# Kernel tuning notes

Hardware: AMD Instinct MI355X
Metric: run time of the kernel (lower is better)

## Reference

```python
import jax, jax.numpy as jnp
import numpy as np

N_HEADS = 12


def setup_inputs() -> dict:
    key = jax.random.key(0)
    ks = jax.random.split(key, 4)
    B, S, D = 2, 2048, 768
    x = jax.random.normal(ks[0], (B, S, D), dtype=jnp.float32)
    # nn.Linear-style init scale ~ 1/sqrt(D) to keep logits reasonable
    scale = 1.0 / np.sqrt(D)
    Wq = jax.random.normal(ks[1], (D, D), dtype=jnp.float32) * scale
    Wk = jax.random.normal(ks[2], (D, D), dtype=jnp.float32) * scale
    Wv = jax.random.normal(ks[3], (D, D), dtype=jnp.float32) * scale
    bq = jnp.zeros((D,), jnp.float32)
    bk = jnp.zeros((D,), jnp.float32)
    bv = jnp.zeros((D,), jnp.float32)
    mask = jnp.ones((B, S), jnp.int32)
    return {"x": x, "Wq": Wq, "bq": bq, "Wk": Wk, "bk": bk,
            "Wv": Wv, "bv": bv, "mask": mask}


def reference(x, Wq, bq, Wk, bk, Wv, bv, mask):
    B, S, D = x.shape
    H = N_HEADS
    W = D // H
    # q,k,v: (B,S,D) -> (B,H,S,W)
    def proj(Wm, bm):
        return (x @ Wm.T + bm).reshape(B, S, H, W).transpose(0, 2, 1, 3)
    q, k, v = proj(Wq, bq), proj(Wk, bk), proj(Wv, bv)
    scores = jnp.einsum("bhsw,bhtw->bhst", q, k) / jnp.sqrt(
        jnp.asarray(W, x.dtype))
    # mask: (B,S) -> broadcast over query positions; 0 -> -1e20
    scores = jnp.where(mask[:, None, None, :] == 0,
                       jnp.asarray(-1e20, scores.dtype), scores)
    attn = jax.nn.softmax(scores, axis=-1)  # (B,H,S,S)
    # dropout p=0.0 (eval) -> identity
    ctx = jnp.einsum("bhst,bhtw->bhsw", attn, v)
    hidden = ctx.transpose(0, 2, 1, 3).reshape(B, S, D)
    return hidden
```

## Files before the change

### kernel.cpp

```cpp
#include <hip/hip_runtime.h>
#include <hip/hip_bf16.h>
#include <stdint.h>


typedef __attribute__((ext_vector_type(8))) short bf16x8;
typedef __attribute__((ext_vector_type(4))) float f32x4;
typedef __attribute__((ext_vector_type(16))) float f32x16;
typedef __attribute__((ext_vector_type(8))) unsigned short u16x8;

#define MFMA16(a, b, c) __builtin_amdgcn_mfma_f32_16x16x32_bf16((a), (b), (c), 0, 0, 0)
#define MFMA32(a, b, c) __builtin_amdgcn_mfma_f32_32x32x16_bf16((a), (b), (c), 0, 0, 0)
#define SWZ(row, colb) ((colb) ^ (((row) & 7) << 4))

union U32x4BF {
  unsigned u[4];
  bf16x8 v;
};

__device__ __forceinline__ void gl_lds16(const void* g, void* l) {
  __builtin_amdgcn_global_load_lds(
      (__attribute__((address_space(1))) void*)const_cast<void*>(g),
      (__attribute__((address_space(3))) void*)l, 16, 0, 0);
}

__device__ __forceinline__ unsigned short f2bf(float x) {
  unsigned int v = __float_as_uint(x);
  return (unsigned short)((v + 0x7fffu + ((v >> 16) & 1u)) >> 16);
}

__global__ __launch_bounds__(256) void cvt_all(
    const float* __restrict__ x, const float* __restrict__ wq,
    const float* __restrict__ wk, const float* __restrict__ wv,
    unsigned short* __restrict__ xb, unsigned short* __restrict__ wb) {
  int i = blockIdx.x * 256 + threadIdx.x;
  const float* s;
  unsigned short* d;
  int off;
  if (i < 393216)      { s = x;  d = xb;            off = i; }
  else if (i < 466944) { s = wq; d = wb;            off = i - 393216; }
  else if (i < 540672) { s = wk; d = wb + 589824;   off = i - 466944; }
  else                 { s = wv; d = wb + 1179648;  off = i - 540672; }
  const float4* sp = (const float4*)s + (size_t)off * 2;
  float4 a = sp[0], b2 = sp[1];
  u16x8 o;
  o[0] = f2bf(a.x); o[1] = f2bf(a.y); o[2] = f2bf(a.z); o[3] = f2bf(a.w);
  o[4] = f2bf(b2.x); o[5] = f2bf(b2.y); o[6] = f2bf(b2.z); o[7] = f2bf(b2.w);
  *((u16x8*)d + off) = o;
}

__global__ __launch_bounds__(256) void proj_gemm(
    const unsigned short* __restrict__ xb, const unsigned short* __restrict__ wb,
    const float* __restrict__ bq, const float* __restrict__ bk, const float* __restrict__ bv,
    unsigned short* __restrict__ qw, unsigned short* __restrict__ kw,
    unsigned short* __restrict__ vw) {
  __shared__ __align__(16) char psmem[49152];
  const int t = threadIdx.x, lane = t & 63, wave = t >> 6;
  const int lo = lane & 15, hi = lane >> 4;
  const int wr = wave >> 1, wc = wave & 1;
  const int mbase = blockIdx.x * 128;
  const int wsel = blockIdx.y / 6;
  const int nbase = (blockIdx.y % 6) * 128;
  const char* xc = (const char*)xb;
  const char* wmc = (const char*)(wb + (size_t)wsel * 589824);

  const int pp0 = t * 16, pp1 = t * 16 + 4096;
  const int ar0 = pp0 >> 7, ac0 = (pp0 & 127) ^ ((ar0 & 7) << 4);
  const int am0 = ((ac0 >> 6) << 6) + ar0, ak0 = ac0 & 63;
  const int ar1 = pp1 >> 7, ac1 = (pp1 & 127) ^ ((ar1 & 7) << 4);
  const int am1 = ((ac1 >> 6) << 6) + ar1, ak1 = ac1 & 63;

#define PSTAGE(IT, BUF)                                                          \
  do {                                                                           \
    int it_ = (IT);                                                              \
    char* lb = psmem + (BUF) * 16384;                                            \
    gl_lds16(xc + (size_t)(mbase + am0) * 1536 + it_ * 64 + ak0, lb + pp0);      \
    gl_lds16(xc + (size_t)(mbase + am1) * 1536 + it_ * 64 + ak1, lb + pp1);      \
    gl_lds16(wmc + (size_t)(nbase + am0) * 1536 + it_ * 64 + ak0, lb + 8192 + pp0); \
    gl_lds16(wmc + (size_t)(nbase + am1) * 1536 + it_ * 64 + ak1, lb + 8192 + pp1); \
  } while (0)

  f32x4 acc[4][4];
#pragma unroll
  for (int i = 0; i < 4; i++)
#pragma unroll
    for (int j = 0; j < 4; j++) acc[i][j] = (f32x4){0.f, 0.f, 0.f, 0.f};

  const int axor = (lo & 7) << 4;
  PSTAGE(0, 0);
  int cur = 0, nxt = 1;
  for (int it = 0; it < 24; ++it) {
    if (it < 23) {
      PSTAGE(it + 1, nxt);
      asm volatile("s_waitcnt vmcnt(4)" ::: "memory");
    } else {
      asm volatile("s_waitcnt vmcnt(0)" ::: "memory");
    }
    __builtin_amdgcn_s_barrier();
    const char* lA = psmem + cur * 16384;
    const char* lB = lA + 8192;

    bf16x8 af[4], bf[4];
#pragma unroll
    for (int mf = 0; mf < 4; mf++)
      af[mf] = *(const bf16x8*)(lA + (mf * 16 + lo) * 128 + ((wr * 64 + hi * 16) ^ axor));
#pragma unroll
    for (int nf = 0; nf < 4; nf++)
      bf[nf] = *(const bf16x8*)(lB + (nf * 16 + lo) * 128 + ((wc * 64 + hi * 16) ^ axor));

    __builtin_amdgcn_s_setprio(1);
    if (wsel == 2) {
#pragma unroll
      for (int mf = 0; mf < 4; mf++)
#pragma unroll
        for (int nf = 0; nf < 4; nf++) acc[mf][nf] = MFMA16(bf[nf], af[mf], acc[mf][nf]);
    } else {
#pragma unroll
      for (int mf = 0; mf < 4; mf++)
#pragma unroll
        for (int nf = 0; nf < 4; nf++) acc[mf][nf] = MFMA16(af[mf], bf[nf], acc[mf][nf]);
    }
    __builtin_amdgcn_s_setprio(0);
    cur = nxt;
    nxt = (nxt == 2) ? 0 : nxt + 1;
  }
#undef PSTAGE

  const float QSCALE = 0.125f * 1.44269504089f;
  if (wsel == 2) {
#pragma unroll
    for (int nf = 0; nf < 4; nf++) {
#pragma unroll
      for (int mf = 0; mf < 4; mf++) {
#pragma unroll
        for (int r = 0; r < 4; r++) {
          int n = nbase + wc * 64 + nf * 16 + hi * 4 + r;
          int m = mbase + wr * 64 + mf * 16 + lo;
          int b_ = m >> 11, s = m & 2047;
          int h = n >> 6, wcol = n & 63;
          float val = acc[mf][nf][r] + bv[n];
          vw[(((size_t)b_ * 12 + h) * 64 + wcol) * 2048 + s] = f2bf(val);
        }
      }
    }
  } else {
    const float* bias = (wsel == 0) ? bq : bk;
#pragma unroll
    for (int nf = 0; nf < 4; nf++) {
      int n = nbase + wc * 64 + nf * 16 + lo;
      float bv_ = bias[n];
      int h = n >> 6, wcol = n & 63;
#pragma unroll
      for (int mf = 0; mf < 4; mf++) {
#pragma unroll
        for (int r = 0; r < 4; r++) {
          int m = mbase + wr * 64 + mf * 16 + hi * 4 + r;
          int b_ = m >> 11, s = m & 2047;
          float val = acc[mf][nf][r] + bv_;
          size_t bhh = (size_t)b_ * 12 + h;
          if (wsel == 0)
            qw[(bhh * 2048 + s) * 64 + wcol] = f2bf(val * QSCALE);
          else
            kw[(bhh * 2048 + s) * 64 + wcol] = f2bf(val);
        }
      }
    }
  }
}

__global__ __launch_bounds__(256) void attn_kernel(
    const unsigned short* __restrict__ qw, const unsigned short* __restrict__ kw,
    const unsigned short* __restrict__ vw, const int* __restrict__ mask,
    float* __restrict__ out) {
  __shared__ __align__(16) char smem[49920];
  const int t = threadIdx.x, lane = t & 63, wave = t >> 6;
  const int wq = wave >> 1, wk = wave & 1;
  const int l31 = lane & 31, hl = lane >> 5;
  const int qb = blockIdx.x, bh = blockIdx.y;
  const int b = bh / 12, hh = bh - b * 12;

  {
    const int* mb = mask + (size_t)b * 2048 + t * 8;
    int4 a0 = *(const int4*)mb;
    int4 a1 = *(const int4*)(mb + 4);
    unsigned by = (unsigned)(a0.x != 0) | ((unsigned)(a0.y != 0) << 1) |
                  ((unsigned)(a0.z != 0) << 2) | ((unsigned)(a0.w != 0) << 3) |
                  ((unsigned)(a1.x != 0) << 4) | ((unsigned)(a1.y != 0) << 5) |
                  ((unsigned)(a1.z != 0) << 6) | ((unsigned)(a1.w != 0) << 7);
    smem[49152 + t] = (char)by;
  }
  asm volatile("s_waitcnt lgkmcnt(0)" ::: "memory");

  bf16x8 qv[4];
  {
    int qrow = qb * 64 + wq * 32 + l31;
    const char* qp = (const char*)qw + ((size_t)bh * 2048 + qrow) * 128 + hl * 16;
#pragma unroll
    for (int s = 0; s < 4; s++) qv[s] = *(const bf16x8*)(qp + s * 32);
  }

  const char* kbaseg = (const char*)kw + (size_t)bh * 262144;
  const char* vbaseg = (const char*)vw + (size_t)bh * 262144;

  const int p0 = t * 16, p1 = t * 16 + 4096;
  const int r0 = p0 >> 9, c0 = (p0 >> 7) & 3, o0 = (p0 & 127) ^ ((r0 & 7) << 4);
  const int ks0 = (c0 * 16 + r0) * 128 + o0, vs0 = (c0 * 16 + r0) * 4096 + o0;
  const int r1 = p1 >> 9, c1 = (p1 >> 7) & 3, o1 = (p1 & 127) ^ ((r1 & 7) << 4);
  const int ks1 = (c1 * 16 + r1) * 128 + o1, vs1 = (c1 * 16 + r1) * 4096 + o1;

#define STAGE(IT, BUF)                                                     \
  do {                                                                     \
    int it_ = (IT);                                                        \
    char* kb = smem + (BUF) * 16384;                                       \
    gl_lds16(kbaseg + (size_t)it_ * 8192 + ks0, kb + p0);                  \
    gl_lds16(kbaseg + (size_t)it_ * 8192 + ks1, kb + p1);                  \
    gl_lds16(vbaseg + (size_t)it_ * 128 + vs0, kb + 8192 + p0);            \
    gl_lds16(vbaseg + (size_t)it_ * 128 + vs1, kb + 8192 + p1);            \
  } while (0)

  f32x16 oacc[2];
#pragma unroll
  for (int wh = 0; wh < 2; wh++)
#pragma unroll
    for (int g = 0; g < 16; g++) oacc[wh][g] = 0.f;
  float lacc = 0.f;

  const int kbl = (l31 & 15) * 512 + (wk * 2 + (l31 >> 4)) * 128;
  const int rxor = (l31 & 7) << 4;
  const int hl16 = hl * 16;

  STAGE(0, 0);
  int cur = 0, nxt = 1;
  for (int it = 0; it < 32; ++it) {
    if (it < 31) {
      STAGE(it + 1, nxt);
      asm volatile("s_waitcnt vmcnt(4)" ::: "memory");
    } else {
      asm volatile("s_waitcnt vmcnt(0)" ::: "memory");
    }
    __builtin_amdgcn_s_barrier();

    const char* lKc = smem + cur * 16384;
    const char* lVc = lKc + 8192;

    f32x16 sc;
#pragma unroll
    for (int g = 0; g < 16; g++) sc[g] = 0.f;
    __builtin_amdgcn_s_setprio(1);
#pragma unroll
    for (int s = 0; s < 4; s++) {
      bf16x8 kf = *(const bf16x8*)(lKc + kbl + ((s * 32 + hl16) ^ rxor));
      sc = MFMA32(kf, qv[s], sc);
    }
    __builtin_amdgcn_s_setprio(0);

    unsigned long long bal = *(const unsigned long long*)(smem + 49152 + it * 8);
    if (bal != ~0ull) {
#pragma unroll
      for (int g = 0; g < 16; g++) {
        int key = wk * 32 + 4 * hl + (g & 3) + 8 * (g >> 2);
        if (!((bal >> key) & 1)) sc[g] = -30000.f;
      }
    }

    float e[16];
#pragma unroll
    for (int g = 0; g < 16; g++)
      asm("v_exp_f32 %0, %1" : "=v"(e[g]) : "v"(sc[g]));
    lacc += (((e[0] + e[1]) + (e[2] + e[3])) + ((e[4] + e[5]) + (e[6] + e[7]))) +
            (((e[8] + e[9]) + (e[10] + e[11])) + ((e[12] + e[13]) + (e[14] + e[15])));
    unsigned pk[4][2];
#pragma unroll
    for (int m = 0; m < 4; m++) {
      asm("v_cvt_pk_bf16_f32 %0, %1, %2" : "=v"(pk[m][0]) : "v"(e[4 * m]), "v"(e[4 * m + 1]));
      asm("v_cvt_pk_bf16_f32 %0, %1, %2" : "=v"(pk[m][1]) : "v"(e[4 * m + 2]), "v"(e[4 * m + 3]));
    }
    U32x4BF apv[2];
#pragma unroll
    for (int sp = 0; sp < 2; sp++)
#pragma unroll
      for (int cp = 0; cp < 2; cp++) {
        unsigned xx = pk[2 * sp][cp], yy = pk[2 * sp + 1][cp];
        asm("v_permlane32_swap_b32 %0, %1" : "+v"(xx), "+v"(yy));
        apv[sp].u[cp] = xx;
        apv[sp].u[2 + cp] = yy;
      }

    __builtin_amdgcn_s_setprio(1);
#pragma unroll
    for (int wh = 0; wh < 2; wh++) {
      int vbl = (l31 & 15) * 512 + (wh * 2 + (l31 >> 4)) * 128;
#pragma unroll
      for (int sp = 0; sp < 2; sp++) {
        bf16x8 vf = *(const bf16x8*)(lVc + vbl + ((wk * 64 + sp * 32 + hl16) ^ rxor));
        oacc[wh] = MFMA32(apv[sp].v, vf, oacc[wh]);
      }
    }
    __builtin_amdgcn_s_setprio(0);
    cur = nxt;
    nxt = (nxt == 2) ? 0 : nxt + 1;
  }

  lacc += __shfl_xor(lacc, 32);
  if (lane < 32)
    *(float*)(smem + 49408 + (wk * 64 + wq * 32 + l31) * 4) = lacc;
  if (wk == 1) {
#pragma unroll
    for (int wh = 0; wh < 2; wh++) {
      int vrow = wh * 32 + l31;
#pragma unroll
      for (int m = 0; m < 4; m++) {
        f32x4 part = (f32x4){oacc[wh][4 * m], oacc[wh][4 * m + 1],
                             oacc[wh][4 * m + 2], oacc[wh][4 * m + 3]};
        *(f32x4*)(smem + wq * 8192 + vrow * 128 + SWZ(vrow, hl * 16 + m * 32)) = part;
      }
    }
  }
  __syncthreads();
  if (wk == 0) {
    float linv[16];
#pragma unroll
    for (int g = 0; g < 16; g++) {
      int qrow = 4 * hl + (g & 3) + 8 * (g >> 2);
      float l0 = *(const float*)(smem + 49408 + (wq * 32 + qrow) * 4);
      float l1 = *(const float*)(smem + 49408 + (64 + wq * 32 + qrow) * 4);
      linv[g] = __builtin_amdgcn_rcpf(l0 + l1);
    }
#pragma unroll
    for (int wh = 0; wh < 2; wh++) {
      int vrow = wh * 32 + l31;
#pragma unroll
      for (int m = 0; m < 4; m++) {
        f32x4 part = *(const f32x4*)(smem + wq * 8192 + vrow * 128 + SWZ(vrow, hl * 16 + m * 32));
#pragma unroll
        for (int r = 0; r < 4; r++) {
          int g = 4 * m + r;
          int qrow = 4 * hl + r + 8 * m;
          float val = (oacc[wh][g] + part[r]) * linv[g];
          out[((size_t)b * 2048 + qb * 64 + wq * 32 + qrow) * 768 + hh * 64 + wh * 32 + l31] =
              val;
        }
      }
    }
  }
#undef STAGE
}

extern "C" void kernel_launch(void* const* d_in, const int* in_sizes, int n_in,
                              void* d_out, int out_size, void* d_ws, size_t ws_size,
                              hipStream_t stream) {
  (void)in_sizes; (void)n_in; (void)out_size; (void)ws_size;
  const float* x  = (const float*)d_in[0];
  const float* Wq = (const float*)d_in[1];
  const float* bq = (const float*)d_in[2];
  const float* Wk = (const float*)d_in[3];
  const float* bk = (const float*)d_in[4];
  const float* Wv = (const float*)d_in[5];
  const float* bv = (const float*)d_in[6];
  const int* mask = (const int*)d_in[7];
  float* out = (float*)d_out;

  char* ws = (char*)d_ws;
  unsigned short* xb = (unsigned short*)(ws);
  unsigned short* wb = (unsigned short*)(ws + 6291456);
  unsigned short* qw = (unsigned short*)(ws + 9830400);
  unsigned short* kw = (unsigned short*)(ws + 16121856);
  unsigned short* vw = (unsigned short*)(ws + 22413312);

  cvt_all<<<2400, 256, 0, stream>>>(x, Wq, Wk, Wv, xb, wb);
  proj_gemm<<<dim3(32, 18), 256, 0, stream>>>(xb, wb, bq, bk, bv, qw, kw, vw);
  attn_kernel<<<dim3(32, 24), 256, 0, stream>>>(qw, kw, vw, mask, out);
}
```

Measured before the change: 86.74 us.

## Deepen prefetch to two stages and compute softmax row sums via MFMA

Both the projection GEMM and the attention kernel now prefetch two tiles ahead in a three-buffer ring, with pointer-increment addressing and an extra barrier at the end of each iteration to protect buffer reuse. The attention loop is manually unrolled by three so buffer indices are compile-time constants. Per-row softmax denominators are now accumulated with an MFMA against a ones vector instead of 16 scalar adds plus a cross-lane shuffle. The aim is to hide more load latency and move VALU work onto the matrix unit, at the cost of an extra barrier per iteration and bf16-rounded exponentials in the denominator sum.

```diff
diff --git a/kernel.cpp b/kernel.cpp
--- a/kernel.cpp
+++ b/kernel.cpp
@@ -69,14 +69,19 @@
   const int ar1 = pp1 >> 7, ac1 = (pp1 & 127) ^ ((ar1 & 7) << 4);
   const int am1 = ((ac1 >> 6) << 6) + ar1, ak1 = ac1 & 63;
 
-#define PSTAGE(IT, BUF)                                                          \
-  do {                                                                           \
-    int it_ = (IT);                                                              \
-    char* lb = psmem + (BUF) * 16384;                                            \
-    gl_lds16(xc + (size_t)(mbase + am0) * 1536 + it_ * 64 + ak0, lb + pp0);      \
-    gl_lds16(xc + (size_t)(mbase + am1) * 1536 + it_ * 64 + ak1, lb + pp1);      \
-    gl_lds16(wmc + (size_t)(nbase + am0) * 1536 + it_ * 64 + ak0, lb + 8192 + pp0); \
-    gl_lds16(wmc + (size_t)(nbase + am1) * 1536 + it_ * 64 + ak1, lb + 8192 + pp1); \
+  const char* xa0 = xc + (size_t)(mbase + am0) * 1536 + ak0;
+  const char* xa1 = xc + (size_t)(mbase + am1) * 1536 + ak1;
+  const char* wa0 = wmc + (size_t)(nbase + am0) * 1536 + ak0;
+  const char* wa1 = wmc + (size_t)(nbase + am1) * 1536 + ak1;
+
+#define PSTAGE(BUF)                              \
+  do {                                           \
+    char* lb = psmem + (BUF) * 16384;            \
+    gl_lds16(xa0, lb + pp0);                     \
+    gl_lds16(xa1, lb + pp1);                     \
+    gl_lds16(wa0, lb + 8192 + pp0);              \
+    gl_lds16(wa1, lb + 8192 + pp1);              \
+    xa0 += 64; xa1 += 64; wa0 += 64; wa1 += 64;  \
   } while (0)
 
   f32x4 acc[4][4];
@@ -86,11 +91,15 @@
     for (int j = 0; j < 4; j++) acc[i][j] = (f32x4){0.f, 0.f, 0.f, 0.f};
 
   const int axor = (lo & 7) << 4;
-  PSTAGE(0, 0);
-  int cur = 0, nxt = 1;
+  PSTAGE(0);
+  PSTAGE(1);
+  int cur = 0, sb = 2;
+#pragma unroll 1
   for (int it = 0; it < 24; ++it) {
-    if (it < 23) {
-      PSTAGE(it + 1, nxt);
+    if (it < 22) {
+      PSTAGE(sb);
+      asm volatile("s_waitcnt vmcnt(8)" ::: "memory");
+    } else if (it == 22) {
       asm volatile("s_waitcnt vmcnt(4)" ::: "memory");
     } else {
       asm volatile("s_waitcnt vmcnt(0)" ::: "memory");
@@ -120,8 +129,9 @@
         for (int nf = 0; nf < 4; nf++) acc[mf][nf] = MFMA16(af[mf], bf[nf], acc[mf][nf]);
     }
     __builtin_amdgcn_s_setprio(0);
-    cur = nxt;
-    nxt = (nxt == 2) ? 0 : nxt + 1;
+    __builtin_amdgcn_s_barrier();
+    cur = (cur == 2) ? 0 : cur + 1;
+    sb = (sb == 2) ? 0 : sb + 1;
   }
 #undef PSTAGE
 
@@ -171,7 +181,7 @@
     const unsigned short* __restrict__ qw, const unsigned short* __restrict__ kw,
     const unsigned short* __restrict__ vw, const int* __restrict__ mask,
     float* __restrict__ out) {
-  __shared__ __align__(16) char smem[49920];
+  __shared__ __align__(16) char smem[49664];
   const int t = threadIdx.x, lane = t & 63, wave = t >> 6;
   const int wq = wave >> 1, wk = wave & 1;
   const int l31 = lane & 31, hl = lane >> 5;
@@ -198,112 +208,116 @@
     for (int s = 0; s < 4; s++) qv[s] = *(const bf16x8*)(qp + s * 32);
   }
 
-  const char* kbaseg = (const char*)kw + (size_t)bh * 262144;
-  const char* vbaseg = (const char*)vw + (size_t)bh * 262144;
-
   const int p0 = t * 16, p1 = t * 16 + 4096;
   const int r0 = p0 >> 9, c0 = (p0 >> 7) & 3, o0 = (p0 & 127) ^ ((r0 & 7) << 4);
-  const int ks0 = (c0 * 16 + r0) * 128 + o0, vs0 = (c0 * 16 + r0) * 4096 + o0;
   const int r1 = p1 >> 9, c1 = (p1 >> 7) & 3, o1 = (p1 & 127) ^ ((r1 & 7) << 4);
-  const int ks1 = (c1 * 16 + r1) * 128 + o1, vs1 = (c1 * 16 + r1) * 4096 + o1;
-
-#define STAGE(IT, BUF)                                                     \
-  do {                                                                     \
-    int it_ = (IT);                                                        \
-    char* kb = smem + (BUF) * 16384;                                       \
-    gl_lds16(kbaseg + (size_t)it_ * 8192 + ks0, kb + p0);                  \
-    gl_lds16(kbaseg + (size_t)it_ * 8192 + ks1, kb + p1);                  \
-    gl_lds16(vbaseg + (size_t)it_ * 128 + vs0, kb + 8192 + p0);            \
-    gl_lds16(vbaseg + (size_t)it_ * 128 + vs1, kb + 8192 + p1);            \
+
+  const char* kp0 = (const char*)kw + (size_t)bh * 262144 + (c0 * 16 + r0) * 128 + o0;
+  const char* kp1 = (const char*)kw + (size_t)bh * 262144 + (c1 * 16 + r1) * 128 + o1;
+  const char* vp0 = (const char*)vw + (size_t)bh * 262144 + (size_t)(c0 * 16 + r0) * 4096 + o0;
+  const char* vp1 = (const char*)vw + (size_t)bh * 262144 + (size_t)(c1 * 16 + r1) * 4096 + o1;
+
+#define STAGEP(BUF_)                              \
+  do {                                            \
+    char* kb_ = smem + (BUF_) * 16384;            \
+    gl_lds16(kp0, kb_ + p0);                      \
+    gl_lds16(kp1, kb_ + p1);                      \
+    gl_lds16(vp0, kb_ + 8192 + p0);               \
+    gl_lds16(vp1, kb_ + 8192 + p1);               \
+    kp0 += 8192; kp1 += 8192; vp0 += 128; vp1 += 128; \
   } while (0)
 
-  f32x16 oacc[2];
+  f32x16 oacc[2], lsacc;
 #pragma unroll
   for (int wh = 0; wh < 2; wh++)
 #pragma unroll
     for (int g = 0; g < 16; g++) oacc[wh][g] = 0.f;
-  float lacc = 0.f;
+#pragma unroll
+  for (int g = 0; g < 16; g++) lsacc[g] = 0.f;
+  U32x4BF onesv;
+  onesv.u[0] = onesv.u[1] = onesv.u[2] = onesv.u[3] = 0x3F803F80u;
 
   const int kbl = (l31 & 15) * 512 + (wk * 2 + (l31 >> 4)) * 128;
   const int rxor = (l31 & 7) << 4;
   const int hl16 = hl * 16;
 
-  STAGE(0, 0);
-  int cur = 0, nxt = 1;
-  for (int it = 0; it < 32; ++it) {
-    if (it < 31) {
-      STAGE(it + 1, nxt);
-      asm volatile("s_waitcnt vmcnt(4)" ::: "memory");
-    } else {
-      asm volatile("s_waitcnt vmcnt(0)" ::: "memory");
-    }
-    __builtin_amdgcn_s_barrier();
-
-    const char* lKc = smem + cur * 16384;
-    const char* lVc = lKc + 8192;
-
-    f32x16 sc;
-#pragma unroll
-    for (int g = 0; g < 16; g++) sc[g] = 0.f;
-    __builtin_amdgcn_s_setprio(1);
-#pragma unroll
-    for (int s = 0; s < 4; s++) {
-      bf16x8 kf = *(const bf16x8*)(lKc + kbl + ((s * 32 + hl16) ^ rxor));
-      sc = MFMA32(kf, qv[s], sc);
-    }
-    __builtin_amdgcn_s_setprio(0);
-
-    unsigned long long bal = *(const unsigned long long*)(smem + 49152 + it * 8);
-    if (bal != ~0ull) {
+  STAGEP(0);
+  STAGEP(1);
+
+#define BODY(IT_, BUF_, DOSTAGE_, SBUF_, VMW_)                                         \
+  {                                                                                    \
+    if (DOSTAGE_) STAGEP(SBUF_);                                                       \
+    asm volatile("s_waitcnt vmcnt(" #VMW_ ")" ::: "memory");                           \
+    __builtin_amdgcn_s_barrier();                                                      \
+    const char* lKc_ = smem + (BUF_) * 16384;                                          \
+    const char* lVc_ = lKc_ + 8192;                                                    \
+    f32x16 sc_;                                                                        \
+    _Pragma("unroll") for (int g = 0; g < 16; g++) sc_[g] = 0.f;                       \
+    __builtin_amdgcn_s_setprio(1);                                                     \
+    _Pragma("unroll") for (int s = 0; s < 4; s++) {                                    \
+      bf16x8 kf_ = *(const bf16x8*)(lKc_ + kbl + ((s * 32 + hl16) ^ rxor));            \
+      sc_ = MFMA32(kf_, qv[s], sc_);                                                   \
+    }                                                                                  \
+    __builtin_amdgcn_s_setprio(0);                                                     \
+    unsigned long long bal_ = *(const unsigned long long*)(smem + 49152 + (IT_) * 8);  \
+    if (bal_ != ~0ull) {                                                               \
+      _Pragma("unroll") for (int g = 0; g < 16; g++) {                                 \
+        int key_ = wk * 32 + 4 * hl + (g & 3) + 8 * (g >> 2);                          \
+        if (!((bal_ >> key_) & 1)) sc_[g] = -30000.f;                                  \
+      }                                                                                \
+    }                                                                                  \
+    float e_[16];                                                                      \
+    _Pragma("unroll") for (int g = 0; g < 16; g++)                                     \
+        asm("v_exp_f32 %0, %1" : "=v"(e_[g]) : "v"(sc_[g]));                           \
+    unsigned pk_[4][2];                                                                \
+    _Pragma("unroll") for (int m = 0; m < 4; m++) {                                    \
+      asm("v_cvt_pk_bf16_f32 %0, %1, %2"                                               \
+          : "=v"(pk_[m][0]) : "v"(e_[4 * m]), "v"(e_[4 * m + 1]));                     \
+      asm("v_cvt_pk_bf16_f32 %0, %1, %2"                                               \
+          : "=v"(pk_[m][1]) : "v"(e_[4 * m + 2]), "v"(e_[4 * m + 3]));                 \
+    }                                                                                  \
+    U32x4BF apv_[2];                                                                   \
+    _Pragma("unroll") for (int sp = 0; sp < 2; sp++)                                   \
+        _Pragma("unroll") for (int cp = 0; cp < 2; cp++) {                             \
+      unsigned xx_ = pk_[2 * sp][cp], yy_ = pk_[2 * sp + 1][cp];                       \
+      asm("v_permlane32_swap_b32 %0, %1" : "+v"(xx_), "+v"(yy_));                      \
+      apv_[sp].u[cp] = xx_;                                                            \
+      apv_[sp].u[2 + cp] = yy_;                                                        \
+    }                                                                                  \
+    __builtin_amdgcn_s_setprio(1);                                                     \
+    lsacc = MFMA32(apv_[0].v, onesv.v, lsacc);                                         \
+    lsacc = MFMA32(apv_[1].v, onesv.v, lsacc);                                         \
+    _Pragma("unroll") for (int wh = 0; wh < 2; wh++) {                                 \
+      int vbl_ = (l31 & 15) * 512 + (wh * 2 + (l31 >> 4)) * 128;                       \
+      _Pragma("unroll") for (int sp = 0; sp < 2; sp++) {                               \
+        bf16x8 vf_ =                                                                   \
+            *(const bf16x8*)(lVc_ + vbl_ + ((wk * 64 + sp * 32 + hl16) ^ rxor));       \
+        oacc[wh] = MFMA32(apv_[sp].v, vf_, oacc[wh]);                                  \
+      }                                                                                \
+    }                                                                                  \
+    __builtin_amdgcn_s_setprio(0);                                                     \
+    __builtin_amdgcn_s_barrier();         \
+  }
+
+#pragma unroll 1
+  for (int itb = 0; itb < 30; itb += 3) {
+    BODY(itb, 0, 1, 2, 8);
+    BODY(itb + 1, 1, 1, 0, 8);
+    BODY(itb + 2, 2, 1, 1, 8);
+  }
+  BODY(30, 0, 0, 0, 4);
+  BODY(31, 1, 0, 0, 0);
+#undef BODY
+#undef STAGEP
+
+  if (wk == 1) {
+    if (l31 == 0) {
 #pragma unroll
       for (int g = 0; g < 16; g++) {
-        int key = wk * 32 + 4 * hl + (g & 3) + 8 * (g >> 2);
-        if (!((bal >> key) & 1)) sc[g] = -30000.f;
-      }
-    }
-
-    float e[16];
-#pragma unroll
-    for (int g = 0; g < 16; g++)
-      asm("v_exp_f32 %0, %1" : "=v"(e[g]) : "v"(sc[g]));
-    lacc += (((e[0] + e[1]) + (e[2] + e[3])) + ((e[4] + e[5]) + (e[6] + e[7]))) +
-            (((e[8] + e[9]) + (e[10] + e[11])) + ((e[12] + e[13]) + (e[14] + e[15])));
-    unsigned pk[4][2];
-#pragma unroll
-    for (int m = 0; m < 4; m++) {
-      asm("v_cvt_pk_bf16_f32 %0, %1, %2" : "=v"(pk[m][0]) : "v"(e[4 * m]), "v"(e[4 * m + 1]));
-      asm("v_cvt_pk_bf16_f32 %0, %1, %2" : "=v"(pk[m][1]) : "v"(e[4 * m + 2]), "v"(e[4 * m + 3]));
-    }
-    U32x4BF apv[2];
-#pragma unroll
-    for (int sp = 0; sp < 2; sp++)
-#pragma unroll
-      for (int cp = 0; cp < 2; cp++) {
-        unsigned xx = pk[2 * sp][cp], yy = pk[2 * sp + 1][cp];
-        asm("v_permlane32_swap_b32 %0, %1" : "+v"(xx), "+v"(yy));
-        apv[sp].u[cp] = xx;
-        apv[sp].u[2 + cp] = yy;
-      }
-
-    __builtin_amdgcn_s_setprio(1);
-#pragma unroll
-    for (int wh = 0; wh < 2; wh++) {
-      int vbl = (l31 & 15) * 512 + (wh * 2 + (l31 >> 4)) * 128;
-#pragma unroll
-      for (int sp = 0; sp < 2; sp++) {
-        bf16x8 vf = *(const bf16x8*)(lVc + vbl + ((wk * 64 + sp * 32 + hl16) ^ rxor));
-        oacc[wh] = MFMA32(apv[sp].v, vf, oacc[wh]);
-      }
-    }
-    __builtin_amdgcn_s_setprio(0);
-    cur = nxt;
-    nxt = (nxt == 2) ? 0 : nxt + 1;
-  }
-
-  lacc += __shfl_xor(lacc, 32);
-  if (lane < 32)
-    *(float*)(smem + 49408 + (wk * 64 + wq * 32 + l31) * 4) = lacc;
-  if (wk == 1) {
+        int qrow = 4 * hl + (g & 3) + 8 * (g >> 2);
+        *(float*)(smem + 49408 + (wq * 32 + qrow) * 4) = lsacc[g];
+      }
+    }
 #pragma unroll
     for (int wh = 0; wh < 2; wh++) {
       int vrow = wh * 32 + l31;
@@ -321,9 +335,8 @@
 #pragma unroll
     for (int g = 0; g < 16; g++) {
       int qrow = 4 * hl + (g & 3) + 8 * (g >> 2);
-      float l0 = *(const float*)(smem + 49408 + (wq * 32 + qrow) * 4);
-      float l1 = *(const float*)(smem + 49408 + (64 + wq * 32 + qrow) * 4);
-      linv[g] = __builtin_amdgcn_rcpf(l0 + l1);
+      float l1 = *(const float*)(smem + 49408 + (wq * 32 + qrow) * 4);
+      linv[g] = __builtin_amdgcn_rcpf(lsacc[g] + l1);
     }
 #pragma unroll
     for (int wh = 0; wh < 2; wh++) {
@@ -342,7 +355,6 @@
       }
     }
   }
-#undef STAGE
 }
 
 extern "C" void kernel_launch(void* const* d_in, const int* in_sizes, int n_in,
```

Result: faster. 84.25 us (-2.9%).

## Pre-swizzle K/V into MFMA fragment layout and load directly to registers

Applied to the files above, without the earlier changes.

The projection GEMM now writes K and V in a tiled layout that matches the 32x32 MFMA operand fragments. This lets the attention kernel load K and V straight from global memory into registers with prefetching, and drops the LDS staging, barriers and the larger shared allocation. The projection GEMM also gets a deeper prefetch (two stages ahead with an extra barrier) and incremented address pointers. The intent is to remove LDS traffic and synchronisation from the attention loop and to raise occupancy. The cost is uncoalesced-style global loads that depend on L2 reuse, since the K/V tiles are no longer shared across the waves of a block.

```diff
diff --git a/kernel.cpp b/kernel.cpp
--- a/kernel.cpp
+++ b/kernel.cpp
@@ -51,8 +51,8 @@
 __global__ __launch_bounds__(256) void proj_gemm(
     const unsigned short* __restrict__ xb, const unsigned short* __restrict__ wb,
     const float* __restrict__ bq, const float* __restrict__ bk, const float* __restrict__ bv,
-    unsigned short* __restrict__ qw, unsigned short* __restrict__ kw,
-    unsigned short* __restrict__ vw) {
+    unsigned short* __restrict__ qw, unsigned short* __restrict__ kx,
+    unsigned short* __restrict__ vx) {
   __shared__ __align__(16) char psmem[49152];
   const int t = threadIdx.x, lane = t & 63, wave = t >> 6;
   const int lo = lane & 15, hi = lane >> 4;
@@ -69,14 +69,19 @@
   const int ar1 = pp1 >> 7, ac1 = (pp1 & 127) ^ ((ar1 & 7) << 4);
   const int am1 = ((ac1 >> 6) << 6) + ar1, ak1 = ac1 & 63;
 
-#define PSTAGE(IT, BUF)                                                          \
-  do {                                                                           \
-    int it_ = (IT);                                                              \
-    char* lb = psmem + (BUF) * 16384;                                            \
-    gl_lds16(xc + (size_t)(mbase + am0) * 1536 + it_ * 64 + ak0, lb + pp0);      \
-    gl_lds16(xc + (size_t)(mbase + am1) * 1536 + it_ * 64 + ak1, lb + pp1);      \
-    gl_lds16(wmc + (size_t)(nbase + am0) * 1536 + it_ * 64 + ak0, lb + 8192 + pp0); \
-    gl_lds16(wmc + (size_t)(nbase + am1) * 1536 + it_ * 64 + ak1, lb + 8192 + pp1); \
+  const char* xa0 = xc + (size_t)(mbase + am0) * 1536 + ak0;
+  const char* xa1 = xc + (size_t)(mbase + am1) * 1536 + ak1;
+  const char* wa0 = wmc + (size_t)(nbase + am0) * 1536 + ak0;
+  const char* wa1 = wmc + (size_t)(nbase + am1) * 1536 + ak1;
+
+#define PSTAGE(BUF)                              \
+  do {                                           \
+    char* lb = psmem + (BUF) * 16384;            \
+    gl_lds16(xa0, lb + pp0);                     \
+    gl_lds16(xa1, lb + pp1);                     \
+    gl_lds16(wa0, lb + 8192 + pp0);              \
+    gl_lds16(wa1, lb + 8192 + pp1);              \
+    xa0 += 64; xa1 += 64; wa0 += 64; wa1 += 64;  \
   } while (0)
 
   f32x4 acc[4][4];
@@ -86,11 +91,15 @@
     for (int j = 0; j < 4; j++) acc[i][j] = (f32x4){0.f, 0.f, 0.f, 0.f};
 
   const int axor = (lo & 7) << 4;
-  PSTAGE(0, 0);
-  int cur = 0, nxt = 1;
+  PSTAGE(0);
+  PSTAGE(1);
+  int cur = 0, sb = 2;
+#pragma unroll 1
   for (int it = 0; it < 24; ++it) {
-    if (it < 23) {
-      PSTAGE(it + 1, nxt);
+    if (it < 22) {
+      PSTAGE(sb);
+      asm volatile("s_waitcnt vmcnt(8)" ::: "memory");
+    } else if (it == 22) {
       asm volatile("s_waitcnt vmcnt(4)" ::: "memory");
     } else {
       asm volatile("s_waitcnt vmcnt(0)" ::: "memory");
@@ -120,8 +129,9 @@
         for (int nf = 0; nf < 4; nf++) acc[mf][nf] = MFMA16(af[mf], bf[nf], acc[mf][nf]);
     }
     __builtin_amdgcn_s_setprio(0);
-    cur = nxt;
-    nxt = (nxt == 2) ? 0 : nxt + 1;
+    __builtin_amdgcn_s_barrier();
+    cur = (cur == 2) ? 0 : cur + 1;
+    sb = (sb == 2) ? 0 : sb + 1;
   }
 #undef PSTAGE
 
@@ -136,9 +146,13 @@
           int n = nbase + wc * 64 + nf * 16 + hi * 4 + r;
           int m = mbase + wr * 64 + mf * 16 + lo;
           int b_ = m >> 11, s = m & 2047;
-          int h = n >> 6, wcol = n & 63;
+          int h = n >> 6, w = n & 63;
           float val = acc[mf][nf][r] + bv[n];
-          vw[(((size_t)b_ * 12 + h) * 64 + wcol) * 2048 + s] = f2bf(val);
+          size_t bhh = (size_t)b_ * 12 + h;
+          size_t idx = bhh * 131072 + (size_t)(s >> 5) * 2048 + (size_t)((w >> 5) & 1) * 1024 +
+                       (size_t)((s >> 4) & 1) * 512 +
+                       (size_t)((w & 31) + 32 * ((s >> 3) & 1)) * 8 + (s & 7);
+          vx[idx] = f2bf(val);
         }
       }
     }
@@ -157,10 +171,14 @@
           int b_ = m >> 11, s = m & 2047;
           float val = acc[mf][nf][r] + bv_;
           size_t bhh = (size_t)b_ * 12 + h;
-          if (wsel == 0)
+          if (wsel == 0) {
             qw[(bhh * 2048 + s) * 64 + wcol] = f2bf(val * QSCALE);
-          else
-            kw[(bhh * 2048 + s) * 64 + wcol] = f2bf(val);
+          } else {
+            int d = wcol;
+            size_t idx = bhh * 131072 + (size_t)(s >> 5) * 2048 + (size_t)(d >> 4) * 512 +
+                         (size_t)((s & 31) + 32 * ((d >> 3) & 1)) * 8 + (d & 7);
+            kx[idx] = f2bf(val);
+          }
         }
       }
     }
@@ -168,10 +186,10 @@
 }
 
 __global__ __launch_bounds__(256) void attn_kernel(
-    const unsigned short* __restrict__ qw, const unsigned short* __restrict__ kw,
-    const unsigned short* __restrict__ vw, const int* __restrict__ mask,
+    const unsigned short* __restrict__ qw, const unsigned short* __restrict__ kx,
+    const unsigned short* __restrict__ vx, const int* __restrict__ mask,
     float* __restrict__ out) {
-  __shared__ __align__(16) char smem[49920];
+  __shared__ __align__(16) char smem[17152];
   const int t = threadIdx.x, lane = t & 63, wave = t >> 6;
   const int wq = wave >> 1, wk = wave & 1;
   const int l31 = lane & 31, hl = lane >> 5;
@@ -186,9 +204,10 @@
                   ((unsigned)(a0.z != 0) << 2) | ((unsigned)(a0.w != 0) << 3) |
                   ((unsigned)(a1.x != 0) << 4) | ((unsigned)(a1.y != 0) << 5) |
                   ((unsigned)(a1.z != 0) << 6) | ((unsigned)(a1.w != 0) << 7);
-    smem[49152 + t] = (char)by;
-  }
-  asm volatile("s_waitcnt lgkmcnt(0)" ::: "memory");
+    smem[16384 + t] = (char)by;
+  }
+  __syncthreads();
+  const unsigned balv = *(const unsigned*)(smem + 16384 + (wk * 32 + l31) * 4);
 
   bf16x8 qv[4];
   {
@@ -198,24 +217,8 @@
     for (int s = 0; s < 4; s++) qv[s] = *(const bf16x8*)(qp + s * 32);
   }
 
-  const char* kbaseg = (const char*)kw + (size_t)bh * 262144;
-  const char* vbaseg = (const char*)vw + (size_t)bh * 262144;
-
-  const int p0 = t * 16, p1 = t * 16 + 4096;
-  const int r0 = p0 >> 9, c0 = (p0 >> 7) & 3, o0 = (p0 & 127) ^ ((r0 & 7) << 4);
-  const int ks0 = (c0 * 16 + r0) * 128 + o0, vs0 = (c0 * 16 + r0) * 4096 + o0;
-  const int r1 = p1 >> 9, c1 = (p1 >> 7) & 3, o1 = (p1 & 127) ^ ((r1 & 7) << 4);
-  const int ks1 = (c1 * 16 + r1) * 128 + o1, vs1 = (c1 * 16 + r1) * 4096 + o1;
-
-#define STAGE(IT, BUF)                                                     \
-  do {                                                                     \
-    int it_ = (IT);                                                        \
-    char* kb = smem + (BUF) * 16384;                                       \
-    gl_lds16(kbaseg + (size_t)it_ * 8192 + ks0, kb + p0);                  \
-    gl_lds16(kbaseg + (size_t)it_ * 8192 + ks1, kb + p1);                  \
-    gl_lds16(vbaseg + (size_t)it_ * 128 + vs0, kb + 8192 + p0);            \
-    gl_lds16(vbaseg + (size_t)it_ * 128 + vs1, kb + 8192 + p1);            \
-  } while (0)
+  const char* kp = (const char*)kx + (size_t)bh * 262144 + (size_t)wk * 131072 + lane * 16;
+  const char* vp = (const char*)vx + (size_t)bh * 262144 + (size_t)wk * 131072 + lane * 16;
 
   f32x16 oacc[2];
 #pragma unroll
@@ -224,55 +227,58 @@
     for (int g = 0; g < 16; g++) oacc[wh][g] = 0.f;
   float lacc = 0.f;
 
-  const int kbl = (l31 & 15) * 512 + (wk * 2 + (l31 >> 4)) * 128;
-  const int rxor = (l31 & 7) << 4;
-  const int hl16 = hl * 16;
-
-  STAGE(0, 0);
-  int cur = 0, nxt = 1;
+  bf16x8 ka0 = *(const bf16x8*)(kp);
+  bf16x8 ka1 = *(const bf16x8*)(kp + 1024);
+  bf16x8 ka2 = *(const bf16x8*)(kp + 2048);
+  bf16x8 ka3 = *(const bf16x8*)(kp + 3072);
+  kp += 4096;
+
+#pragma unroll 2
   for (int it = 0; it < 32; ++it) {
-    if (it < 31) {
-      STAGE(it + 1, nxt);
-      asm volatile("s_waitcnt vmcnt(4)" ::: "memory");
-    } else {
-      asm volatile("s_waitcnt vmcnt(0)" ::: "memory");
-    }
-    __builtin_amdgcn_s_barrier();
-
-    const char* lKc = smem + cur * 16384;
-    const char* lVc = lKc + 8192;
+    bf16x8 v00 = *(const bf16x8*)(vp);
+    bf16x8 v01 = *(const bf16x8*)(vp + 1024);
+    bf16x8 v10 = *(const bf16x8*)(vp + 2048);
+    bf16x8 v11 = *(const bf16x8*)(vp + 3072);
+    vp += 4096;
 
     f32x16 sc;
 #pragma unroll
     for (int g = 0; g < 16; g++) sc[g] = 0.f;
     __builtin_amdgcn_s_setprio(1);
-#pragma unroll
-    for (int s = 0; s < 4; s++) {
-      bf16x8 kf = *(const bf16x8*)(lKc + kbl + ((s * 32 + hl16) ^ rxor));
-      sc = MFMA32(kf, qv[s], sc);
-    }
+    sc = MFMA32(ka0, qv[0], sc);
+    sc = MFMA32(ka1, qv[1], sc);
+    sc = MFMA32(ka2, qv[2], sc);
+    sc = MFMA32(ka3, qv[3], sc);
     __builtin_amdgcn_s_setprio(0);
 
-    unsigned long long bal = *(const unsigned long long*)(smem + 49152 + it * 8);
-    if (bal != ~0ull) {
+    ka0 = *(const bf16x8*)(kp);
+    ka1 = *(const bf16x8*)(kp + 1024);
+    ka2 = *(const bf16x8*)(kp + 2048);
+    ka3 = *(const bf16x8*)(kp + 3072);
+    kp += 4096;
+
+    unsigned bal = __builtin_amdgcn_readlane(balv, it);
+    if (bal != 0xFFFFFFFFu) {
 #pragma unroll
       for (int g = 0; g < 16; g++) {
-        int key = wk * 32 + 4 * hl + (g & 3) + 8 * (g >> 2);
+        int key = (g & 3) + 8 * (g >> 2) + 4 * hl;
         if (!((bal >> key) & 1)) sc[g] = -30000.f;
       }
     }
 
-    float e[16];
-#pragma unroll
-    for (int g = 0; g < 16; g++)
-      asm("v_exp_f32 %0, %1" : "=v"(e[g]) : "v"(sc[g]));
-    lacc += (((e[0] + e[1]) + (e[2] + e[3])) + ((e[4] + e[5]) + (e[6] + e[7]))) +
-            (((e[8] + e[9]) + (e[10] + e[11])) + ((e[12] + e[13]) + (e[14] + e[15])));
+#pragma unroll
+    for (int g = 0; g < 16; g++) {
+      float e_;
+      asm("v_exp_f32 %0, %1" : "=v"(e_) : "v"(sc[g]));
+      sc[g] = e_;
+    }
+    lacc += (((sc[0] + sc[1]) + (sc[2] + sc[3])) + ((sc[4] + sc[5]) + (sc[6] + sc[7]))) +
+            (((sc[8] + sc[9]) + (sc[10] + sc[11])) + ((sc[12] + sc[13]) + (sc[14] + sc[15])));
     unsigned pk[4][2];
 #pragma unroll
     for (int m = 0; m < 4; m++) {
-      asm("v_cvt_pk_bf16_f32 %0, %1, %2" : "=v"(pk[m][0]) : "v"(e[4 * m]), "v"(e[4 * m + 1]));
-      asm("v_cvt_pk_bf16_f32 %0, %1, %2" : "=v"(pk[m][1]) : "v"(e[4 * m + 2]), "v"(e[4 * m + 3]));
+      asm("v_cvt_pk_bf16_f32 %0, %1, %2" : "=v"(pk[m][0]) : "v"(sc[4 * m]), "v"(sc[4 * m + 1]));
+      asm("v_cvt_pk_bf16_f32 %0, %1, %2" : "=v"(pk[m][1]) : "v"(sc[4 * m + 2]), "v"(sc[4 * m + 3]));
     }
     U32x4BF apv[2];
 #pragma unroll
@@ -286,23 +292,16 @@
       }
 
     __builtin_amdgcn_s_setprio(1);
-#pragma unroll
-    for (int wh = 0; wh < 2; wh++) {
-      int vbl = (l31 & 15) * 512 + (wh * 2 + (l31 >> 4)) * 128;
-#pragma unroll
-      for (int sp = 0; sp < 2; sp++) {
-        bf16x8 vf = *(const bf16x8*)(lVc + vbl + ((wk * 64 + sp * 32 + hl16) ^ rxor));
-        oacc[wh] = MFMA32(apv[sp].v, vf, oacc[wh]);
-      }
-    }
+    oacc[0] = MFMA32(apv[0].v, v00, oacc[0]);
+    oacc[0] = MFMA32(apv[1].v, v01, oacc[0]);
+    oacc[1] = MFMA32(apv[0].v, v10, oacc[1]);
+    oacc[1] = MFMA32(apv[1].v, v11, oacc[1]);
     __builtin_amdgcn_s_setprio(0);
-    cur = nxt;
-    nxt = (nxt == 2) ? 0 : nxt + 1;
   }
 
   lacc += __shfl_xor(lacc, 32);
   if (lane < 32)
-    *(float*)(smem + 49408 + (wk * 64 + wq * 32 + l31) * 4) = lacc;
+    *(float*)(smem + 16640 + (((wq * 32 + l31) << 1) + wk) * 4) = lacc;
   if (wk == 1) {
 #pragma unroll
     for (int wh = 0; wh < 2; wh++) {
@@ -321,9 +320,8 @@
 #pragma unroll
     for (int g = 0; g < 16; g++) {
       int qrow = 4 * hl + (g & 3) + 8 * (g >> 2);
-      float l0 = *(const float*)(smem + 49408 + (wq * 32 + qrow) * 4);
-      float l1 = *(const float*)(smem + 49408 + (64 + wq * 32 + qrow) * 4);
-      linv[g] = __builtin_amdgcn_rcpf(l0 + l1);
+      float2 lp = *(const float2*)(smem + 16640 + ((wq * 32 + qrow) << 3));
+      linv[g] = __builtin_amdgcn_rcpf(lp.x + lp.y);
     }
 #pragma unroll
     for (int wh = 0; wh < 2; wh++) {
@@ -342,7 +340,6 @@
       }
     }
   }
-#undef STAGE
 }
 
 extern "C" void kernel_launch(void* const* d_in, const int* in_sizes, int n_in,
@@ -363,10 +360,10 @@
   unsigned short* xb = (unsigned short*)(ws);
   unsigned short* wb = (unsigned short*)(ws + 6291456);
   unsigned short* qw = (unsigned short*)(ws + 9830400);
-  unsigned short* kw = (unsigned short*)(ws + 16121856);
-  unsigned short* vw = (unsigned short*)(ws + 22413312);
+  unsigned short* kx = (unsigned short*)(ws + 16121856);
+  unsigned short* vx = (unsigned short*)(ws + 22413312);
 
   cvt_all<<<2400, 256, 0, stream>>>(x, Wq, Wk, Wv, xb, wb);
-  proj_gemm<<<dim3(32, 18), 256, 0, stream>>>(xb, wb, bq, bk, bv, qw, kw, vw);
-  attn_kernel<<<dim3(32, 24), 256, 0, stream>>>(qw, kw, vw, mask, out);
-}
+  proj_gemm<<<dim3(32, 18), 256, 0, stream>>>(xb, wb, bq, bk, bv, qw, kx, vx);
+  attn_kernel<<<dim3(32, 24), 256, 0, stream>>>(qw, kx, vx, mask, out);
+}
```

After: 93.18 us. 7.4% more time.
